# Optimization experiments

Measured on AMD Instinct MI355X. Metric: run time of the kernel, lower is better.

The kernel has to match this reference:

```python
import jax, jax.numpy as jnp
import numpy as np

N, E, P = 50000, 500000, 10000
F_IN, H, C = 128, 256, 1


def gat_conv(x, src, dst, W, a_s, a_d, b):
    # single-head GATConv (PyG): h = x W; e_ij = LeakyReLU(a_s.h_j + a_d.h_i)
    n = x.shape[0]
    h = x @ W                              # [n, out]
    es = h @ a_s                           # [n]
    ed = h @ a_d                           # [n]
    logits = jax.nn.leaky_relu(es[src] + ed[dst], 0.2)   # [E']
    m = jax.ops.segment_max(logits, dst, num_segments=n)
    p = jnp.exp(logits - m[dst])
    denom = jax.ops.segment_sum(p, dst, num_segments=n)
    alpha = p / denom[dst]                 # edge-softmax over incoming edges
    out = jax.ops.segment_sum(h[src] * alpha[:, None], dst, num_segments=n)
    return out + b


def setup_inputs():
    key = jax.random.key(0)
    ks = jax.random.split(key, 14)
    inp = {
        "features": jax.random.normal(ks[0], (N, F_IN), jnp.float32),
        "edge_index": jax.random.randint(ks[1], (2, E), 0, N, dtype=jnp.int32),
        "mask": jax.random.randint(ks[2], (P, 2), 0, N, dtype=jnp.int32),
        "W1": jax.random.normal(ks[3], (F_IN, H), jnp.float32) / np.sqrt(F_IN),
        "a_src1": jax.random.normal(ks[4], (H,), jnp.float32) / np.sqrt(H),
        "a_dst1": jax.random.normal(ks[5], (H,), jnp.float32) / np.sqrt(H),
        "b1": jnp.zeros((H,), jnp.float32),
        "W2": jax.random.normal(ks[6], (H, F_IN), jnp.float32) / np.sqrt(H),
        "a_src2": jax.random.normal(ks[7], (F_IN,), jnp.float32) / np.sqrt(F_IN),
        "a_dst2": jax.random.normal(ks[8], (F_IN,), jnp.float32) / np.sqrt(F_IN),
        "b2": jnp.zeros((F_IN,), jnp.float32),
        "Wl": jax.random.normal(ks[9], (2 * F_IN, C), jnp.float32) / np.sqrt(2 * F_IN),
        "bl": jnp.zeros((C,), jnp.float32),
    }
    return inp


def reference(features, edge_index, mask, W1, a_src1, a_dst1, b1, W2, a_src2, a_dst2, b2, Wl, bl):
    n = features.shape[0]
    loop = jnp.arange(n, dtype=edge_index.dtype)   # PyG add_self_loops=True
    src = jnp.concatenate([edge_index[0], loop])
    dst = jnp.concatenate([edge_index[1], loop])
    h = gat_conv(features, src, dst, W1, a_src1, a_dst1, b1)   # [N, H]
    h = jax.nn.relu(h)                                         # dropout=0.0
    h = gat_conv(h, src, dst, W2, a_src2, a_dst2, b2)          # [N, F_IN]
    mT = mask.T
    p1 = jax.lax.stop_gradient(h[mT[0]])   # .detach() in original
    p2 = jax.lax.stop_gradient(h[mT[1]])
    z = jnp.concatenate([p1, p2], axis=1)  # [P, 2*F_IN]
    return jax.nn.sigmoid(z @ Wl + bl)
```

## Files before the change

### kernel.cpp

```cpp
#include <hip/hip_runtime.h>
#include <hip/hip_bf16.h>
#include <math.h>

#define NN 50000
#define NE 500000
#define NP 10000
#define FIN 128
#define HD 256
#define CAP 64
#define NBG 391

typedef __attribute__((ext_vector_type(8))) short bf16x8;
typedef __attribute__((ext_vector_type(4))) float f32x4;
typedef __attribute__((ext_vector_type(2))) float f32x2;

__device__ inline unsigned short f2bf(float f) {
  unsigned int u = __float_as_uint(f);
  unsigned int r = (u + 0x7fffu + ((u >> 16) & 1u)) >> 16;
  return (unsigned short)r;
}

__device__ inline unsigned int cvtpk_bf16(float lo, float hi) {
  unsigned int r;
  asm("v_cvt_pk_bf16_f32 %0, %1, %2" : "=v"(r) : "v"(lo), "v"(hi));
  return r;
}

__device__ inline float bflo(unsigned int u) { return __uint_as_float(u << 16); }
__device__ inline float bfhi(unsigned int u) { return __uint_as_float(u & 0xffff0000u); }

__device__ inline unsigned char f2fp8(float v) {
  int pk = __builtin_amdgcn_cvt_pk_fp8_f32(v, v, 0, false);
  return (unsigned char)(pk & 0xff);
}

__global__ void init_prep(int* __restrict__ deg,
                          const float* __restrict__ W1, const float* __restrict__ W2,
                          unsigned short* __restrict__ W1T, unsigned short* __restrict__ W2T) {
  int idx = blockIdx.x * 256 + threadIdx.x;
  if (idx < NN) deg[idx] = 0;
  if (idx < FIN * HD) {
    int n = idx / FIN, k = idx - n * FIN;
    W1T[idx] = f2bf(W1[(size_t)k * HD + n]);
    int n2 = idx / HD, k2 = idx - n2 * HD;
    W2T[idx] = f2bf(W2[(size_t)k2 * FIN + n2]);
  }
}

template <int BN, int KTOT>
__global__ __launch_bounds__(512)
void gemm_hist(const float* __restrict__ Aptr, const unsigned short* __restrict__ BT,
               unsigned char* __restrict__ Cptr, const float* __restrict__ a_s,
               const float* __restrict__ a_d, float* __restrict__ es, float* __restrict__ ed,
               int M, const int* __restrict__ dst, int* __restrict__ deg,
               int* __restrict__ rank) {
  if (blockIdx.x >= NBG) {
    int e = (blockIdx.x - NBG) * 512 + threadIdx.x;
    if (e < NE) rank[e] = atomicAdd(&deg[dst[e]], 1);
    return;
  }
  constexpr int LDK = 72;
  constexpr int CN = BN / 2;
  constexpr int NT = CN / 16;
  __shared__ unsigned short As[128][LDK];
  __shared__ unsigned short Bs[BN][LDK];
  __shared__ float esl[128][2];
  __shared__ float edl[128][2];
  const int tid = threadIdx.x;
  const int wave = tid >> 6;
  const int lane = tid & 63;
  const int quad = lane >> 4;
  const int l16 = lane & 15;
  const int wrow = wave >> 1;
  const int wcol = wave & 1;
  const int row0 = blockIdx.x * 128;

  f32x4 acc[2][NT] = {};

  for (int k0 = 0; k0 < KTOT; k0 += 64) {
#pragma unroll
    for (int p = 0; p < 4; p++) {
      int m = p * 32 + (tid >> 4);
      int k4 = (tid & 15) * 4;
      int gr = row0 + m;
      uint2 pk = make_uint2(0u, 0u);
      if (gr < M) {
        float4 v = *(const float4*)(Aptr + (size_t)gr * KTOT + k0 + k4);
        pk.x = cvtpk_bf16(v.x, v.y);
        pk.y = cvtpk_bf16(v.z, v.w);
      }
      *(uint2*)&As[m][k4] = pk;
    }
#pragma unroll
    for (int p = 0; p < BN / 64; p++) {
      int n = p * 64 + (tid >> 3);
      int k8 = (tid & 7) * 8;
      *(uint4*)&Bs[n][k8] = *(const uint4*)(BT + (size_t)n * KTOT + k0 + k8);
    }
    __syncthreads();
#pragma unroll
    for (int ks = 0; ks < 2; ks++) {
      bf16x8 afrag[2];
#pragma unroll
      for (int rt = 0; rt < 2; rt++)
        afrag[rt] = *(const bf16x8*)&As[wrow * 32 + rt * 16 + l16][ks * 32 + quad * 8];
#pragma unroll
      for (int ct = 0; ct < NT; ct++) {
        bf16x8 bfrag = *(const bf16x8*)&Bs[wcol * CN + ct * 16 + l16][ks * 32 + quad * 8];
#pragma unroll
        for (int rt = 0; rt < 2; rt++)
          acc[rt][ct] = __builtin_amdgcn_mfma_f32_16x16x32_bf16(afrag[rt], bfrag, acc[rt][ct], 0, 0, 0);
      }
    }
    __syncthreads();
  }

  float asv[NT], adv[NT];
#pragma unroll
  for (int ct = 0; ct < NT; ct++) {
    asv[ct] = a_s[wcol * CN + ct * 16 + l16];
    adv[ct] = a_d[wcol * CN + ct * 16 + l16];
  }
#pragma unroll
  for (int rt = 0; rt < 2; rt++) {
#pragma unroll
    for (int r = 0; r < 4; r++) {
      int lrow = wrow * 32 + rt * 16 + quad * 4 + r;
      int grow = row0 + lrow;
      bool ok = (grow < M);
      float ps = 0.f, pd = 0.f;
#pragma unroll
      for (int ct = 0; ct < NT; ct++) {
        float v = acc[rt][ct][r];
        ps += v * asv[ct];
        pd += v * adv[ct];
        if (ok) {
          size_t cidx = (size_t)grow * BN + wcol * CN + ct * 16 + l16;
          Cptr[cidx] = f2fp8(v);
        }
      }
#pragma unroll
      for (int off = 1; off < 16; off <<= 1) {
        ps += __shfl_xor(ps, off, 16);
        pd += __shfl_xor(pd, off, 16);
      }
      if (l16 == 0) {
        esl[lrow][wcol] = ps;
        edl[lrow][wcol] = pd;
      }
    }
  }
  __syncthreads();
  if (tid < 128) {
    int grow = row0 + tid;
    if (grow < M) {
      es[grow] = esl[tid][0] + esl[tid][1];
      ed[grow] = edl[tid][0] + edl[tid][1];
    }
  }
}

__global__ void scatter_kernel(const int* __restrict__ src, const int* __restrict__ dst,
                               const int* __restrict__ rank, const int* __restrict__ deg,
                               int* __restrict__ ssrc) {
  int t = blockIdx.x * blockDim.x + threadIdx.x;
  int e = t * 2;
  if (e < NE) {
    int2 d2 = *(const int2*)(dst + e);
    int2 s2 = *(const int2*)(src + e);
    int2 r2 = *(const int2*)(rank + e);
    if (r2.x < CAP - 1) ssrc[d2.x * CAP + r2.x] = s2.x;
    if (r2.y < CAP - 1) ssrc[d2.y * CAP + r2.y] = s2.y;
  } else {
    int i = t - NE / 2;
    if (i < NN) ssrc[i * CAP + min(deg[i], CAP - 1)] = i;
  }
}

template <int BN, int KTOT>
__global__ __launch_bounds__(512)
void gemm2_dots(const unsigned short* __restrict__ Aptr, const unsigned short* __restrict__ BT,
                const float* __restrict__ a_s, const float* __restrict__ a_d,
                const float* __restrict__ wl0, const float* __restrict__ wl1,
                float* __restrict__ es, float* __restrict__ ed,
                float* __restrict__ g0, float* __restrict__ g1, int M) {
  constexpr int LDK = 72;
  constexpr int CN = BN / 2;
  constexpr int NT = CN / 16;
  __shared__ unsigned short As[128][LDK];
  __shared__ unsigned short Bs[BN][LDK];
  __shared__ float esl[128][2];
  __shared__ float edl[128][2];
  __shared__ float g0l[128][2];
  __shared__ float g1l[128][2];
  const int tid = threadIdx.x;
  const int wave = tid >> 6;
  const int lane = tid & 63;
  const int quad = lane >> 4;
  const int l16 = lane & 15;
  const int wrow = wave >> 1;
  const int wcol = wave & 1;
  const int row0 = blockIdx.x * 128;

  f32x4 acc[2][NT] = {};

  for (int k0 = 0; k0 < KTOT; k0 += 64) {
#pragma unroll
    for (int p = 0; p < 4; p++) {
      int m = p * 32 + (tid >> 4);
      int k4 = (tid & 15) * 4;
      int gr = row0 + m;
      uint2 pk = make_uint2(0u, 0u);
      if (gr < M)
        pk = *(const uint2*)(Aptr + (size_t)gr * KTOT + k0 + k4);
      *(uint2*)&As[m][k4] = pk;
    }
#pragma unroll
    for (int p = 0; p < BN / 64; p++) {
      int n = p * 64 + (tid >> 3);
      int k8 = (tid & 7) * 8;
      *(uint4*)&Bs[n][k8] = *(const uint4*)(BT + (size_t)n * KTOT + k0 + k8);
    }
    __syncthreads();
#pragma unroll
    for (int ks = 0; ks < 2; ks++) {
      bf16x8 afrag[2];
#pragma unroll
      for (int rt = 0; rt < 2; rt++)
        afrag[rt] = *(const bf16x8*)&As[wrow * 32 + rt * 16 + l16][ks * 32 + quad * 8];
#pragma unroll
      for (int ct = 0; ct < NT; ct++) {
        bf16x8 bfrag = *(const bf16x8*)&Bs[wcol * CN + ct * 16 + l16][ks * 32 + quad * 8];
#pragma unroll
        for (int rt = 0; rt < 2; rt++)
          acc[rt][ct] = __builtin_amdgcn_mfma_f32_16x16x32_bf16(afrag[rt], bfrag, acc[rt][ct], 0, 0, 0);
      }
    }
    __syncthreads();
  }

  float asv[NT], adv[NT], w0v[NT], w1v[NT];
#pragma unroll
  for (int ct = 0; ct < NT; ct++) {
    int col = wcol * CN + ct * 16 + l16;
    asv[ct] = a_s[col];
    adv[ct] = a_d[col];
    w0v[ct] = wl0[col];
    w1v[ct] = wl1[col];
  }
#pragma unroll
  for (int rt = 0; rt < 2; rt++) {
#pragma unroll
    for (int r = 0; r < 4; r++) {
      int lrow = wrow * 32 + rt * 16 + quad * 4 + r;
      float ps = 0.f, pd = 0.f, p0 = 0.f, p1 = 0.f;
#pragma unroll
      for (int ct = 0; ct < NT; ct++) {
        float v = acc[rt][ct][r];
        ps += v * asv[ct];
        pd += v * adv[ct];
        p0 += v * w0v[ct];
        p1 += v * w1v[ct];
      }
#pragma unroll
      for (int off = 1; off < 16; off <<= 1) {
        ps += __shfl_xor(ps, off, 16);
        pd += __shfl_xor(pd, off, 16);
        p0 += __shfl_xor(p0, off, 16);
        p1 += __shfl_xor(p1, off, 16);
      }
      if (l16 == 0) {
        esl[lrow][wcol] = ps;
        edl[lrow][wcol] = pd;
        g0l[lrow][wcol] = p0;
        g1l[lrow][wcol] = p1;
      }
    }
  }
  __syncthreads();
  if (tid < 128) {
    int grow = row0 + tid;
    if (grow < M) {
      es[grow] = esl[tid][0] + esl[tid][1];
      ed[grow] = edl[tid][0] + edl[tid][1];
      g0[grow] = g0l[tid][0] + g0l[tid][1];
      g1[grow] = g1l[tid][0] + g1l[tid][1];
    }
  }
}

__global__ __launch_bounds__(256)
void fused_agg64(const int* __restrict__ deg, const int* __restrict__ ssrc,
                 const float* __restrict__ es, const float* __restrict__ ed,
                 const unsigned char* __restrict__ h, const float* __restrict__ bias,
                 unsigned short* __restrict__ outp, int n) {
  int i = blockIdx.x * 16 + (threadIdx.x >> 4);
  int ls = threadIdx.x & 15;
  if (i >= n) return;
  int s = i * CAP;
  int e = s + min(deg[i] + 1, CAP);
  float edv = ed[i];

  float acc[16] = {};
  float lsum = 0.f;
  const unsigned char* hb = h + ls * 16;
  for (int p0 = s; p0 < e; p0 += 16) {
    int p = p0 + ls;
    int msrc = 0;
    float pv = 0.f;
    if (p < e) {
      msrc = ssrc[p];
      float t = es[msrc] + edv;
      float lg = (t > 0.f) ? t : 0.2f * t;
      pv = __expf(lg);
    }
    lsum += pv;
    int cnt = min(16, e - p0);
    int jfull = cnt & ~3;
    for (int j = 0; j < jfull; j += 4) {
      uint4 r[4];
      float w[4];
#pragma unroll
      for (int u = 0; u < 4; u++) {
        int jj = j + u;
        int sj = __shfl(msrc, jj, 16);
        w[u] = __shfl(pv, jj, 16);
        r[u] = *(const uint4*)(hb + (size_t)sj * HD);
      }
#pragma unroll
      for (int u = 0; u < 4; u++) {
        f32x2 lo, hi;
        lo = __builtin_amdgcn_cvt_pk_f32_fp8(r[u].x, false);
        hi = __builtin_amdgcn_cvt_pk_f32_fp8(r[u].x, true);
        acc[0] += w[u] * lo.x; acc[1] += w[u] * lo.y; acc[2] += w[u] * hi.x; acc[3] += w[u] * hi.y;
        lo = __builtin_amdgcn_cvt_pk_f32_fp8(r[u].y, false);
        hi = __builtin_amdgcn_cvt_pk_f32_fp8(r[u].y, true);
        acc[4] += w[u] * lo.x; acc[5] += w[u] * lo.y; acc[6] += w[u] * hi.x; acc[7] += w[u] * hi.y;
        lo = __builtin_amdgcn_cvt_pk_f32_fp8(r[u].z, false);
        hi = __builtin_amdgcn_cvt_pk_f32_fp8(r[u].z, true);
        acc[8] += w[u] * lo.x; acc[9] += w[u] * lo.y; acc[10] += w[u] * hi.x; acc[11] += w[u] * hi.y;
        lo = __builtin_amdgcn_cvt_pk_f32_fp8(r[u].w, false);
        hi = __builtin_amdgcn_cvt_pk_f32_fp8(r[u].w, true);
        acc[12] += w[u] * lo.x; acc[13] += w[u] * lo.y; acc[14] += w[u] * hi.x; acc[15] += w[u] * hi.y;
      }
    }
    if (jfull < cnt) {
      uint4 r[4];
      float w[4];
#pragma unroll
      for (int u = 0; u < 4; u++) {
        int jj = jfull + u;
        bool ok = jj < cnt;
        int jc = ok ? jj : 0;
        int sj = __shfl(msrc, jc, 16);
        float wr = __shfl(pv, jc, 16);
        w[u] = ok ? wr : 0.f;
        r[u] = *(const uint4*)(hb + (size_t)sj * HD);
      }
#pragma unroll
      for (int u = 0; u < 4; u++) {
        f32x2 lo, hi;
        lo = __builtin_amdgcn_cvt_pk_f32_fp8(r[u].x, false);
        hi = __builtin_amdgcn_cvt_pk_f32_fp8(r[u].x, true);
        acc[0] += w[u] * lo.x; acc[1] += w[u] * lo.y; acc[2] += w[u] * hi.x; acc[3] += w[u] * hi.y;
        lo = __builtin_amdgcn_cvt_pk_f32_fp8(r[u].y, false);
        hi = __builtin_amdgcn_cvt_pk_f32_fp8(r[u].y, true);
        acc[4] += w[u] * lo.x; acc[5] += w[u] * lo.y; acc[6] += w[u] * hi.x; acc[7] += w[u] * hi.y;
        lo = __builtin_amdgcn_cvt_pk_f32_fp8(r[u].z, false);
        hi = __builtin_amdgcn_cvt_pk_f32_fp8(r[u].z, true);
        acc[8] += w[u] * lo.x; acc[9] += w[u] * lo.y; acc[10] += w[u] * hi.x; acc[11] += w[u] * hi.y;
        lo = __builtin_amdgcn_cvt_pk_f32_fp8(r[u].w, false);
        hi = __builtin_amdgcn_cvt_pk_f32_fp8(r[u].w, true);
        acc[12] += w[u] * lo.x; acc[13] += w[u] * lo.y; acc[14] += w[u] * hi.x; acc[15] += w[u] * hi.y;
      }
    }
  }
#pragma unroll
  for (int off = 8; off; off >>= 1) lsum += __shfl_xor(lsum, off, 16);
  float invd = 1.0f / lsum;
  float4 b0 = *(const float4*)(bias + ls * 16 + 0);
  float4 b1 = *(const float4*)(bias + ls * 16 + 4);
  float4 b2 = *(const float4*)(bias + ls * 16 + 8);
  float4 b3 = *(const float4*)(bias + ls * 16 + 12);
  float v0 = fmaxf(acc[0] * invd + b0.x, 0.f),  v1 = fmaxf(acc[1] * invd + b0.y, 0.f);
  float v2 = fmaxf(acc[2] * invd + b0.z, 0.f),  v3 = fmaxf(acc[3] * invd + b0.w, 0.f);
  float v4 = fmaxf(acc[4] * invd + b1.x, 0.f),  v5 = fmaxf(acc[5] * invd + b1.y, 0.f);
  float v6 = fmaxf(acc[6] * invd + b1.z, 0.f),  v7 = fmaxf(acc[7] * invd + b1.w, 0.f);
  float v8 = fmaxf(acc[8] * invd + b2.x, 0.f),  v9 = fmaxf(acc[9] * invd + b2.y, 0.f);
  float va = fmaxf(acc[10] * invd + b2.z, 0.f), vb = fmaxf(acc[11] * invd + b2.w, 0.f);
  float vc = fmaxf(acc[12] * invd + b3.x, 0.f), vd = fmaxf(acc[13] * invd + b3.y, 0.f);
  float ve = fmaxf(acc[14] * invd + b3.z, 0.f), vf = fmaxf(acc[15] * invd + b3.w, 0.f);
  unsigned short* ob = outp + (size_t)i * HD + ls * 16;
  *(uint4*)(ob) = make_uint4(cvtpk_bf16(v0, v1), cvtpk_bf16(v2, v3),
                             cvtpk_bf16(v4, v5), cvtpk_bf16(v6, v7));
  *(uint4*)(ob + 8) = make_uint4(cvtpk_bf16(v8, v9), cvtpk_bf16(va, vb),
                                 cvtpk_bf16(vc, vd), cvtpk_bf16(ve, vf));
}

__global__ __launch_bounds__(256)
void predict_l2(const int* __restrict__ deg, const int* __restrict__ ssrc,
                const float* __restrict__ es, const float* __restrict__ ed,
                const float* __restrict__ g0, const float* __restrict__ g1,
                const float* __restrict__ b2, const int* __restrict__ mask,
                const float* __restrict__ Wl, const float* __restrict__ bl,
                float* __restrict__ out, int P) {
  int pair = blockIdx.x * 8 + (threadIdx.x >> 5);
  if (pair >= P) return;
  int l32 = threadIdx.x & 31;
  int hf = l32 >> 4;
  int ls = l32 & 15;
  int i = mask[pair * 2 + hf];
  int s = i * CAP;
  int cnt = min(deg[i] + 1, CAP);
  float edv = ed[i];
  const float* g = hf ? g1 : g0;

  float lsum = 0.f, accg = 0.f;
  for (int k = ls; k < cnt; k += 16) {
    int m = ssrc[s + k];
    float t = es[m] + edv;
    float lg = (t > 0.f) ? t : 0.2f * t;
    float pv = __expf(lg);
    lsum += pv;
    accg += pv * g[m];
  }
  float accb = 0.f;
  const float* wv = Wl + hf * FIN + ls * 8;
  const float* bv = b2 + ls * 8;
#pragma unroll
  for (int q = 0; q < 8; q++) accb += bv[q] * wv[q];
#pragma unroll
  for (int off = 8; off; off >>= 1) {
    lsum += __shfl_xor(lsum, off, 16);
    accg += __shfl_xor(accg, off, 16);
    accb += __shfl_xor(accb, off, 16);
  }
  float zs = accg / lsum + accb;
  float othr = __shfl_xor(zs, 16, 32);
  if (l32 == 0) {
    float z = zs + othr + bl[0];
    out[pair] = 1.0f / (1.0f + expf(-z));
  }
}

extern "C" void kernel_launch(void* const* d_in, const int* in_sizes, int n_in,
                              void* d_out, int out_size, void* d_ws, size_t ws_size,
                              hipStream_t stream) {
  const float* features = (const float*)d_in[0];
  const int* edge_index = (const int*)d_in[1];
  const int* mask       = (const int*)d_in[2];
  const float* W1     = (const float*)d_in[3];
  const float* a_src1 = (const float*)d_in[4];
  const float* a_dst1 = (const float*)d_in[5];
  const float* b1     = (const float*)d_in[6];
  const float* W2     = (const float*)d_in[7];
  const float* a_src2 = (const float*)d_in[8];
  const float* a_dst2 = (const float*)d_in[9];
  const float* b2     = (const float*)d_in[10];
  const float* Wl     = (const float*)d_in[11];
  const float* bl     = (const float*)d_in[12];
  float* out = (float*)d_out;

  const int* src = edge_index;
  const int* dst = edge_index + NE;

  char* ws = (char*)d_ws;
  size_t off = 0;
  auto alloc = [&](size_t bytes) {
    void* p = ws + off;
    off += (bytes + 255) & ~(size_t)255;
    return p;
  };
  unsigned char* h1q = (unsigned char*)alloc((size_t)NN * HD);
  unsigned short* x2b = (unsigned short*)alloc((size_t)NN * HD * 2);
  unsigned short* W1T = (unsigned short*)alloc((size_t)HD * FIN * 2);
  unsigned short* W2T = (unsigned short*)alloc((size_t)FIN * HD * 2);
  float* es_buf  = (float*)alloc((size_t)NN * 4);
  float* ed_buf  = (float*)alloc((size_t)NN * 4);
  float* g0_buf  = (float*)alloc((size_t)NN * 4);
  float* g1_buf  = (float*)alloc((size_t)NN * 4);
  int* deg       = (int*)alloc((size_t)NN * 4);
  int* rank      = (int*)alloc((size_t)NE * 4);
  int* ssrc      = (int*)alloc((size_t)NN * CAP * 4);
  (void)ws_size; (void)in_sizes; (void)n_in; (void)out_size;

  const int nblk_n256 = (NN + 255) / 256;
  const int nblk_hist = (NE + 511) / 512;
  const int nblk_scat = (NE / 2 + NN + 255) / 256;

  init_prep<<<nblk_n256, 256, 0, stream>>>(deg, W1, W2, W1T, W2T);
  gemm_hist<HD, FIN><<<NBG + nblk_hist, 512, 0, stream>>>(
      features, W1T, h1q, a_src1, a_dst1, es_buf, ed_buf, NN, dst, deg, rank);
  scatter_kernel<<<nblk_scat, 256, 0, stream>>>(src, dst, rank, deg, ssrc);
  fused_agg64<<<(NN + 15) / 16, 256, 0, stream>>>(
      deg, ssrc, es_buf, ed_buf, h1q, b1, x2b, NN);
  gemm2_dots<FIN, HD><<<(NN + 127) / 128, 512, 0, stream>>>(
      x2b, W2T, a_src2, a_dst2, Wl, Wl + FIN, es_buf, ed_buf, g0_buf, g1_buf, NN);
  predict_l2<<<(NP + 7) / 8, 256, 0, stream>>>(
      deg, ssrc, es_buf, ed_buf, g0_buf, g1_buf, b2, mask, Wl, bl, out, NP);
}
```

Before: 182.8 us.

## Pack source score with neighbor index and precompute bias-weight dot product

The scatter kernel now stores each edge's layer-1 source score next to its source index as an int2. The layer-1 aggregation then reads both in one load instead of doing a dependent random gather of es. The b2·Wl dot product is computed once in init_prep instead of per pair in predict_l2. In exchange, the neighbor table doubles in size and scatter does an extra random es gather; predict_l2 now reads 8-byte entries to use only the index.

```diff
diff --git a/kernel.cpp b/kernel.cpp
--- a/kernel.cpp
+++ b/kernel.cpp
@@ -36,7 +36,9 @@
 
 __global__ void init_prep(int* __restrict__ deg,
                           const float* __restrict__ W1, const float* __restrict__ W2,
-                          unsigned short* __restrict__ W1T, unsigned short* __restrict__ W2T) {
+                          unsigned short* __restrict__ W1T, unsigned short* __restrict__ W2T,
+                          const float* __restrict__ b2, const float* __restrict__ Wl,
+                          float* __restrict__ bw) {
   int idx = blockIdx.x * 256 + threadIdx.x;
   if (idx < NN) deg[idx] = 0;
   if (idx < FIN * HD) {
@@ -44,6 +46,15 @@
     W1T[idx] = f2bf(W1[(size_t)k * HD + n]);
     int n2 = idx / HD, k2 = idx - n2 * HD;
     W2T[idx] = f2bf(W2[(size_t)k2 * FIN + n2]);
+  }
+  if (blockIdx.x == 0 && threadIdx.x < 128) {
+    int w = threadIdx.x >> 6;
+    int lane = threadIdx.x & 63;
+    int f = lane * 2;
+    float p = b2[f] * Wl[w * FIN + f] + b2[f + 1] * Wl[w * FIN + f + 1];
+#pragma unroll
+    for (int off = 32; off; off >>= 1) p += __shfl_xor(p, off, 64);
+    if (lane == 0) bw[w] = p;
   }
 }
 
@@ -162,18 +173,18 @@
 
 __global__ void scatter_kernel(const int* __restrict__ src, const int* __restrict__ dst,
                                const int* __restrict__ rank, const int* __restrict__ deg,
-                               int* __restrict__ ssrc) {
+                               const float* __restrict__ es, int2* __restrict__ sv) {
   int t = blockIdx.x * blockDim.x + threadIdx.x;
   int e = t * 2;
   if (e < NE) {
     int2 d2 = *(const int2*)(dst + e);
     int2 s2 = *(const int2*)(src + e);
     int2 r2 = *(const int2*)(rank + e);
-    if (r2.x < CAP - 1) ssrc[d2.x * CAP + r2.x] = s2.x;
-    if (r2.y < CAP - 1) ssrc[d2.y * CAP + r2.y] = s2.y;
+    if (r2.x < CAP - 1) sv[d2.x * CAP + r2.x] = make_int2(s2.x, __float_as_int(es[s2.x]));
+    if (r2.y < CAP - 1) sv[d2.y * CAP + r2.y] = make_int2(s2.y, __float_as_int(es[s2.y]));
   } else {
     int i = t - NE / 2;
-    if (i < NN) ssrc[i * CAP + min(deg[i], CAP - 1)] = i;
+    if (i < NN) sv[i * CAP + min(deg[i], CAP - 1)] = make_int2(i, __float_as_int(es[i]));
   }
 }
 
@@ -290,8 +301,8 @@
 }
 
 __global__ __launch_bounds__(256)
-void fused_agg64(const int* __restrict__ deg, const int* __restrict__ ssrc,
-                 const float* __restrict__ es, const float* __restrict__ ed,
+void fused_agg64(const int* __restrict__ deg, const int2* __restrict__ sv,
+                 const float* __restrict__ ed,
                  const unsigned char* __restrict__ h, const float* __restrict__ bias,
                  unsigned short* __restrict__ outp, int n) {
   int i = blockIdx.x * 16 + (threadIdx.x >> 4);
@@ -309,8 +320,9 @@
     int msrc = 0;
     float pv = 0.f;
     if (p < e) {
-      msrc = ssrc[p];
-      float t = es[msrc] + edv;
+      int2 q = sv[p];
+      msrc = q.x;
+      float t = __int_as_float(q.y) + edv;
       float lg = (t > 0.f) ? t : 0.2f * t;
       pv = __expf(lg);
     }
@@ -398,12 +410,11 @@
 }
 
 __global__ __launch_bounds__(256)
-void predict_l2(const int* __restrict__ deg, const int* __restrict__ ssrc,
+void predict_l2(const int* __restrict__ deg, const int2* __restrict__ sv,
                 const float* __restrict__ es, const float* __restrict__ ed,
                 const float* __restrict__ g0, const float* __restrict__ g1,
-                const float* __restrict__ b2, const int* __restrict__ mask,
-                const float* __restrict__ Wl, const float* __restrict__ bl,
-                float* __restrict__ out, int P) {
+                const float* __restrict__ bw, const int* __restrict__ mask,
+                const float* __restrict__ bl, float* __restrict__ out, int P) {
   int pair = blockIdx.x * 8 + (threadIdx.x >> 5);
   if (pair >= P) return;
   int l32 = threadIdx.x & 31;
@@ -417,25 +428,19 @@
 
   float lsum = 0.f, accg = 0.f;
   for (int k = ls; k < cnt; k += 16) {
-    int m = ssrc[s + k];
+    int m = sv[s + k].x;
     float t = es[m] + edv;
     float lg = (t > 0.f) ? t : 0.2f * t;
     float pv = __expf(lg);
     lsum += pv;
     accg += pv * g[m];
   }
-  float accb = 0.f;
-  const float* wv = Wl + hf * FIN + ls * 8;
-  const float* bv = b2 + ls * 8;
-#pragma unroll
-  for (int q = 0; q < 8; q++) accb += bv[q] * wv[q];
 #pragma unroll
   for (int off = 8; off; off >>= 1) {
     lsum += __shfl_xor(lsum, off, 16);
     accg += __shfl_xor(accg, off, 16);
-    accb += __shfl_xor(accb, off, 16);
-  }
-  float zs = accg / lsum + accb;
+  }
+  float zs = accg / lsum + bw[hf];
   float othr = __shfl_xor(zs, 16, 32);
   if (l32 == 0) {
     float z = zs + othr + bl[0];
@@ -479,23 +484,24 @@
   float* ed_buf  = (float*)alloc((size_t)NN * 4);
   float* g0_buf  = (float*)alloc((size_t)NN * 4);
   float* g1_buf  = (float*)alloc((size_t)NN * 4);
+  float* bw_buf  = (float*)alloc(256);
   int* deg       = (int*)alloc((size_t)NN * 4);
   int* rank      = (int*)alloc((size_t)NE * 4);
-  int* ssrc      = (int*)alloc((size_t)NN * CAP * 4);
+  int2* sv       = (int2*)alloc((size_t)NN * CAP * 8);
   (void)ws_size; (void)in_sizes; (void)n_in; (void)out_size;
 
   const int nblk_n256 = (NN + 255) / 256;
   const int nblk_hist = (NE + 511) / 512;
   const int nblk_scat = (NE / 2 + NN + 255) / 256;
 
-  init_prep<<<nblk_n256, 256, 0, stream>>>(deg, W1, W2, W1T, W2T);
+  init_prep<<<nblk_n256, 256, 0, stream>>>(deg, W1, W2, W1T, W2T, b2, Wl, bw_buf);
   gemm_hist<HD, FIN><<<NBG + nblk_hist, 512, 0, stream>>>(
       features, W1T, h1q, a_src1, a_dst1, es_buf, ed_buf, NN, dst, deg, rank);
-  scatter_kernel<<<nblk_scat, 256, 0, stream>>>(src, dst, rank, deg, ssrc);
+  scatter_kernel<<<nblk_scat, 256, 0, stream>>>(src, dst, rank, deg, es_buf, sv);
   fused_agg64<<<(NN + 15) / 16, 256, 0, stream>>>(
-      deg, ssrc, es_buf, ed_buf, h1q, b1, x2b, NN);
+      deg, sv, ed_buf, h1q, b1, x2b, NN);
   gemm2_dots<FIN, HD><<<(NN + 127) / 128, 512, 0, stream>>>(
       x2b, W2T, a_src2, a_dst2, Wl, Wl + FIN, es_buf, ed_buf, g0_buf, g1_buf, NN);
   predict_l2<<<(NP + 7) / 8, 256, 0, stream>>>(
-      deg, ssrc, es_buf, ed_buf, g0_buf, g1_buf, b2, mask, Wl, bl, out, NP);
-}
+      deg, sv, es_buf, ed_buf, g0_buf, g1_buf, bw_buf, mask, bl, out, NP);
+}
```

Result: no change. 182.9 us (+0.0%).
